# Optimization experiments

Measured on AMD Instinct MI355X. Metric: run time of the kernel, lower is better.

Reference implementation:

```python
import jax, jax.numpy as jnp
import numpy as np

B, L, H = 16, 512, 1024
HEADS, HEAD_SIZE = 12, 64
NEG = 1e12


def sinusoidal_position_embedding(seq_len, output_dim):
    pos = jnp.arange(seq_len, dtype=jnp.float32)[:, None]
    idx = jnp.arange(output_dim // 2, dtype=jnp.float32)
    freqs = pos * jnp.power(10000.0, -2.0 * idx / output_dim)  # [L, D/2]
    emb = jnp.stack([jnp.sin(freqs), jnp.cos(freqs)], axis=-1)  # [L, D/2, 2]
    return emb.reshape(seq_len, output_dim)  # interleaved sin/cos, [L, D]


def setup_inputs() -> dict:
    key = jax.random.key(0)
    k1, k2, k3 = jax.random.split(key, 3)
    inputs = jax.random.normal(k1, (B, L, H), dtype=jnp.float32)
    mask = jnp.ones((B, L), dtype=jnp.int32)
    W = jax.random.normal(k2, (H, HEADS * HEAD_SIZE * 2), dtype=jnp.float32) / np.sqrt(H)
    b = jax.random.normal(k3, (HEADS * HEAD_SIZE * 2,), dtype=jnp.float32) * 0.01
    pos_emb = sinusoidal_position_embedding(L, HEAD_SIZE)  # [L, HEAD_SIZE]
    return {"inputs": inputs, "mask": mask, "W": W, "b": b, "pos_emb": pos_emb}


def rotate_half_interleaved(x):
    # stack([-x[..., 1::2], x[..., ::2]], -1).reshape(x.shape)
    x2 = jnp.stack([-x[..., 1::2], x[..., ::2]], axis=-1)
    return x2.reshape(x.shape)


def reference(inputs, mask, W, b, pos_emb):
    bsz, seq_len, _ = inputs.shape
    d = pos_emb.shape[-1]
    heads = W.shape[1] // (2 * d)
    out = inputs @ W + b                       # [B, L, heads*2d]
    out = out.reshape(bsz, seq_len, heads, 2 * d)
    qw, kw = out[..., :d], out[..., d:]        # [B, L, heads, d]
    cos_pos = jnp.repeat(pos_emb[:, 1::2], 2, axis=-1)[None, :, None, :]  # [1,L,1,d]
    sin_pos = jnp.repeat(pos_emb[:, 0::2], 2, axis=-1)[None, :, None, :]
    qw = qw * cos_pos + rotate_half_interleaved(qw) * sin_pos
    kw = kw * cos_pos + rotate_half_interleaved(kw) * sin_pos
    logits = jnp.einsum('bmhd,bnhd->bhmn', qw, kw)  # [B, heads, L, L]
    pad = mask.astype(logits.dtype)[:, None, None, :] * mask.astype(logits.dtype)[:, None, :, None]
    # torch code: expand of mask[:,None,None,:] -> applies along last axis only;
    # replicate exactly: pad_mask broadcasts mask over the query axis.
    pad_mask = jnp.broadcast_to(mask.astype(logits.dtype)[:, None, None, :], logits.shape)
    logits = logits * pad_mask - (1.0 - pad_mask) * NEG
    tril = jnp.tril(jnp.ones((seq_len, seq_len), dtype=logits.dtype), -1)
    logits = logits - tril[None, None, :, :] * NEG
    return logits / jnp.sqrt(jnp.array(d, dtype=logits.dtype))
```

## Files before the change

kernel.cpp:

```cpp
#include <hip/hip_runtime.h>

#define BB 16
#define LL 512
#define HH 1024
#define HEADS 12
#define DD 64
#define N1 1536
#define M1 8192
#define NEGC 1e12f

typedef short bf16x8 __attribute__((ext_vector_type(8)));
typedef float f32x4 __attribute__((ext_vector_type(4)));

typedef const __attribute__((address_space(1))) unsigned int glob_u32;
typedef __attribute__((address_space(3))) unsigned int lds_u32;

__device__ __forceinline__ void gl_lds16(const unsigned short* g, unsigned short* l) {
    __builtin_amdgcn_global_load_lds((glob_u32*)g, (lds_u32*)l, 16, 0, 0);
}

__device__ __forceinline__ unsigned short f2bf(float f) {
    union { float f; unsigned int u; } v; v.f = f;
    unsigned int u = v.u;
    return (unsigned short)((u + 0x7fffu + ((u >> 16) & 1u)) >> 16);
}

__global__ __launch_bounds__(256) void k_conv_x(const float* __restrict__ X,
                                                unsigned short* __restrict__ Xb,
                                                int n4) {
    int i = blockIdx.x * 256 + threadIdx.x;
    if (i >= n4) return;
    float4 v = ((const float4*)X)[i];
    ushort4 o;
    o.x = f2bf(v.x); o.y = f2bf(v.y); o.z = f2bf(v.z); o.w = f2bf(v.w);
    ((ushort4*)Xb)[i] = o;
}

__global__ __launch_bounds__(256) void k_trans_w(const float* __restrict__ W,
                                                 unsigned short* __restrict__ Wt) {
    __shared__ float tile[32][33];
    int n0 = blockIdx.x * 32;
    int k0 = blockIdx.y * 32;
    int tx = threadIdx.x;
    int ty = threadIdx.y;
#pragma unroll
    for (int i = 0; i < 4; i++) {
        int k = ty + i * 8;
        tile[k][tx] = W[(size_t)(k0 + k) * N1 + n0 + tx];
    }
    __syncthreads();
#pragma unroll
    for (int i = 0; i < 4; i++) {
        int n = ty + i * 8;
        Wt[(size_t)(n0 + n) * HH + k0 + tx] = f2bf(tile[tx][n]);
    }
}

__global__ __launch_bounds__(256) void k_gemm1_rope(
    const unsigned short* __restrict__ Xb,
    const unsigned short* __restrict__ Wt,
    const float* __restrict__ bias,
    const float* __restrict__ pe,
    unsigned short* __restrict__ Qr,
    unsigned short* __restrict__ Kr)
{
    __shared__ __align__(16) unsigned short As[128 * 32];
    __shared__ __align__(16) unsigned short Bs[128 * 32];
    int m0 = blockIdx.y * 128;
    int n0 = blockIdx.x * 128;
    int tid = threadIdx.x;
    int w  = tid >> 6;
    int ln = tid & 63;
    int lq = ln >> 4;
    int lm = ln & 15;
    int wm = (w & 1) * 64;
    int wn = (w >> 1) * 64;

    int lrow = ln >> 2;
    int lcol = (ln & 3) * 8;
    const unsigned short* ga0 = &Xb[(size_t)(m0 + w * 32 + lrow) * HH + lcol];
    const unsigned short* ga1 = ga0 + (size_t)16 * HH;
    const unsigned short* gb0 = &Wt[(size_t)(n0 + w * 32 + lrow) * HH + lcol];
    const unsigned short* gb1 = gb0 + (size_t)16 * HH;
    unsigned short* la0 = &As[(w * 32) * 32];
    unsigned short* la1 = la0 + 16 * 32;
    unsigned short* lb0 = &Bs[(w * 32) * 32];
    unsigned short* lb1 = lb0 + 16 * 32;

    const unsigned short* pa = &As[(wm + lm) * 32];
    const unsigned short* pb = &Bs[(wn + lm) * 32];

    f32x4 acc[4][4] = {};

    for (int kk = 0; kk < HH; kk += 32) {
        gl_lds16(ga0 + kk, la0);
        gl_lds16(ga1 + kk, la1);
        gl_lds16(gb0 + kk, lb0);
        gl_lds16(gb1 + kk, lb1);
        __syncthreads();

        bf16x8 af[4], bf[4];
#pragma unroll
        for (int t = 0; t < 4; t++) {
            af[t] = *(const bf16x8*)&pa[t * 16 * 32 + lq * 8];
            bf[t] = *(const bf16x8*)&pb[t * 16 * 32 + lq * 8];
        }
#pragma unroll
        for (int ti = 0; ti < 4; ti++)
#pragma unroll
            for (int tj = 0; tj < 4; tj++)
                acc[ti][tj] = __builtin_amdgcn_mfma_f32_16x16x32_bf16(af[ti], bf[tj], acc[ti][tj], 0, 0, 0);
        __syncthreads();
    }

#pragma unroll
    for (int tj = 0; tj < 4; tj++) {
        int n = n0 + wn + tj * 16 + lm;
        float bv = bias[n];
        int h = n >> 7;
        int c = n & 127;
        int j = c & 63;
        int ii = j >> 1;
        bool isK = (c >= 64);
        unsigned short* dst = isK ? Kr : Qr;
#pragma unroll
        for (int ti = 0; ti < 4; ti++) {
#pragma unroll
            for (int r = 0; r < 4; r++) {
                int m = m0 + wm + ti * 16 + lq * 4 + r;
                int l = m & (LL - 1);
                int bidx = m >> 9;
                float v = acc[ti][tj][r] + bv;
                float vp = __shfl_xor(v, 1, 64);
                float2 sc = *(const float2*)&pe[l * 64 + 2 * ii];
                float o = (j & 1) ? (v * sc.y + vp * sc.x) : (v * sc.y - vp * sc.x);
                size_t idx = ((size_t)(bidx * HEADS + h) * LL + l) * DD + j;
                dst[idx] = f2bf(o);
            }
        }
    }
}

__global__ __launch_bounds__(256) void k_gemm2(
    const unsigned short* __restrict__ Qr,
    const unsigned short* __restrict__ Kr,
    const int* __restrict__ mask,
    float* __restrict__ out)
{
    __shared__ __align__(16) unsigned short Qs[64 * 72];
    __shared__ __align__(16) unsigned short Ks[64 * 72];
    int bh = blockIdx.z;
    int b  = bh / HEADS;
    int n0 = blockIdx.x * 64;
    int m0 = blockIdx.y * 64;
    int tid = threadIdx.x;
    int w  = tid >> 6;
    int ln = tid & 63;
    int lq = ln >> 4;
    int lm = ln & 15;
    int mw = (w & 1) * 32;
    int nw = (w >> 1) * 32;

    const unsigned short* Qb = Qr + (size_t)bh * LL * DD;
    const unsigned short* Kb = Kr + (size_t)bh * LL * DD;

    int srow = tid >> 3;
    int scol = (tid & 7) * 8;
#pragma unroll
    for (int p = 0; p < 2; p++) {
        int row = srow + p * 32;
        *(uint4*)&Qs[row * 72 + scol] = *(const uint4*)&Qb[(size_t)(m0 + row) * DD + scol];
        *(uint4*)&Ks[row * 72 + scol] = *(const uint4*)&Kb[(size_t)(n0 + row) * DD + scol];
    }
    __syncthreads();

    f32x4 acc[2][2] = {};
#pragma unroll
    for (int kk = 0; kk < 64; kk += 32) {
        bf16x8 q0 = *(const bf16x8*)&Qs[(mw + lm) * 72 + kk + lq * 8];
        bf16x8 q1 = *(const bf16x8*)&Qs[(mw + 16 + lm) * 72 + kk + lq * 8];
        bf16x8 k0 = *(const bf16x8*)&Ks[(nw + lm) * 72 + kk + lq * 8];
        bf16x8 k1 = *(const bf16x8*)&Ks[(nw + 16 + lm) * 72 + kk + lq * 8];
        acc[0][0] = __builtin_amdgcn_mfma_f32_16x16x32_bf16(k0, q0, acc[0][0], 0, 0, 0);
        acc[0][1] = __builtin_amdgcn_mfma_f32_16x16x32_bf16(k1, q0, acc[0][1], 0, 0, 0);
        acc[1][0] = __builtin_amdgcn_mfma_f32_16x16x32_bf16(k0, q1, acc[1][0], 0, 0, 0);
        acc[1][1] = __builtin_amdgcn_mfma_f32_16x16x32_bf16(k1, q1, acc[1][1], 0, 0, 0);
    }

#pragma unroll
    for (int tm = 0; tm < 2; tm++) {
        int m = m0 + mw + tm * 16 + lm;
#pragma unroll
        for (int tn = 0; tn < 2; tn++) {
            int nb = n0 + nw + tn * 16 + lq * 4;
            int4 mv = *(const int4*)&mask[b * LL + nb];
            float4 val;
            {
                float pm = (float)mv.x; int n = nb;
                val.x = (acc[tm][tn][0] * pm - (1.0f - pm) * NEGC - (n < m ? NEGC : 0.0f)) * 0.125f;
            }
            {
                float pm = (float)mv.y; int n = nb + 1;
                val.y = (acc[tm][tn][1] * pm - (1.0f - pm) * NEGC - (n < m ? NEGC : 0.0f)) * 0.125f;
            }
            {
                float pm = (float)mv.z; int n = nb + 2;
                val.z = (acc[tm][tn][2] * pm - (1.0f - pm) * NEGC - (n < m ? NEGC : 0.0f)) * 0.125f;
            }
            {
                float pm = (float)mv.w; int n = nb + 3;
                val.w = (acc[tm][tn][3] * pm - (1.0f - pm) * NEGC - (n < m ? NEGC : 0.0f)) * 0.125f;
            }
            *(float4*)&out[((size_t)bh * LL + m) * LL + nb] = val;
        }
    }
}

extern "C" void kernel_launch(void* const* d_in, const int* in_sizes, int n_in,
                              void* d_out, int out_size, void* d_ws, size_t ws_size,
                              hipStream_t stream) {
    const float* X    = (const float*)d_in[0];
    const int*   mask = (const int*)d_in[1];
    const float* W    = (const float*)d_in[2];
    const float* bias = (const float*)d_in[3];
    const float* pe   = (const float*)d_in[4];
    float* out = (float*)d_out;

    char* ws = (char*)d_ws;
    unsigned short* Xb = (unsigned short*)ws;
    unsigned short* Wt = (unsigned short*)(ws + 16777216);
    unsigned short* Qr = (unsigned short*)(ws + 16777216 + 3145728);
    unsigned short* Kr = Qr + (size_t)BB * HEADS * LL * DD;

    k_conv_x<<<dim3((M1 * HH / 4 + 255) / 256), dim3(256), 0, stream>>>(X, Xb, M1 * HH / 4);
    k_trans_w<<<dim3(N1 / 32, HH / 32), dim3(32, 8), 0, stream>>>(W, Wt);
    k_gemm1_rope<<<dim3(N1 / 128, M1 / 128), dim3(256), 0, stream>>>(Xb, Wt, bias, pe, Qr, Kr);
    k_gemm2<<<dim3(LL / 64, LL / 64, BB * HEADS), dim3(256), 0, stream>>>(Qr, Kr, mask, out);
}
```

Measured before the change: 327.2 us.

## Transpose gemm1 MFMA output for vectorized RoPE stores; enlarge gemm2 tiles to 128x128

In gemm1 the MFMA operands are swapped so each lane holds four consecutive output columns. RoPE pairs can then be rotated within a lane, removing the cross-lane shuffle and the scalar bf16 stores in favour of ushort4 stores with float4 bias and position-embedding loads. In gemm2 the tile grows from 64x64 to 128x128, with each wave computing a 4x4 block of MFMA tiles and the head dimension split into two LDS halves. This cuts the block count and amortizes the mask load over more outputs, at the cost of more registers per thread and fewer blocks in flight.

```diff
diff --git a/kernel.cpp b/kernel.cpp
--- a/kernel.cpp
+++ b/kernel.cpp
@@ -87,8 +87,8 @@
     unsigned short* lb0 = &Bs[(w * 32) * 32];
     unsigned short* lb1 = lb0 + 16 * 32;
 
-    const unsigned short* pa = &As[(wm + lm) * 32];
-    const unsigned short* pb = &Bs[(wn + lm) * 32];
+    const unsigned short* px = &As[(wm + lm) * 32];
+    const unsigned short* pw = &Bs[(wn + lm) * 32];
 
     f32x4 acc[4][4] = {};
 
@@ -99,44 +99,46 @@
         gl_lds16(gb1 + kk, lb1);
         __syncthreads();
 
-        bf16x8 af[4], bf[4];
+        bf16x8 xf[4], wf[4];
 #pragma unroll
         for (int t = 0; t < 4; t++) {
-            af[t] = *(const bf16x8*)&pa[t * 16 * 32 + lq * 8];
-            bf[t] = *(const bf16x8*)&pb[t * 16 * 32 + lq * 8];
+            xf[t] = *(const bf16x8*)&px[t * 16 * 32 + lq * 8];
+            wf[t] = *(const bf16x8*)&pw[t * 16 * 32 + lq * 8];
         }
 #pragma unroll
         for (int ti = 0; ti < 4; ti++)
 #pragma unroll
             for (int tj = 0; tj < 4; tj++)
-                acc[ti][tj] = __builtin_amdgcn_mfma_f32_16x16x32_bf16(af[ti], bf[tj], acc[ti][tj], 0, 0, 0);
+                acc[ti][tj] = __builtin_amdgcn_mfma_f32_16x16x32_bf16(wf[tj], xf[ti], acc[ti][tj], 0, 0, 0);
         __syncthreads();
     }
 
 #pragma unroll
     for (int tj = 0; tj < 4; tj++) {
-        int n = n0 + wn + tj * 16 + lm;
-        float bv = bias[n];
-        int h = n >> 7;
-        int c = n & 127;
-        int j = c & 63;
-        int ii = j >> 1;
+        int nb = n0 + wn + tj * 16 + lq * 4;
+        float4 b4 = *(const float4*)&bias[nb];
+        int h  = nb >> 7;
+        int c  = nb & 127;
+        int jb = c & 63;
         bool isK = (c >= 64);
         unsigned short* dst = isK ? Kr : Qr;
+        size_t hoff = (size_t)h * LL * DD + jb;
 #pragma unroll
         for (int ti = 0; ti < 4; ti++) {
-#pragma unroll
-            for (int r = 0; r < 4; r++) {
-                int m = m0 + wm + ti * 16 + lq * 4 + r;
-                int l = m & (LL - 1);
-                int bidx = m >> 9;
-                float v = acc[ti][tj][r] + bv;
-                float vp = __shfl_xor(v, 1, 64);
-                float2 sc = *(const float2*)&pe[l * 64 + 2 * ii];
-                float o = (j & 1) ? (v * sc.y + vp * sc.x) : (v * sc.y - vp * sc.x);
-                size_t idx = ((size_t)(bidx * HEADS + h) * LL + l) * DD + j;
-                dst[idx] = f2bf(o);
-            }
+            int m = m0 + wm + ti * 16 + lm;
+            int l = m & (LL - 1);
+            int bidx = m >> 9;
+            float4 p4 = *(const float4*)&pe[l * 64 + jb];
+            float v0 = acc[ti][tj][0] + b4.x;
+            float v1 = acc[ti][tj][1] + b4.y;
+            float v2 = acc[ti][tj][2] + b4.z;
+            float v3 = acc[ti][tj][3] + b4.w;
+            ushort4 st;
+            st.x = f2bf(v0 * p4.y - v1 * p4.x);
+            st.y = f2bf(v1 * p4.y + v0 * p4.x);
+            st.z = f2bf(v2 * p4.w - v3 * p4.z);
+            st.w = f2bf(v3 * p4.w + v2 * p4.z);
+            *(ushort4*)&dst[(size_t)bidx * HEADS * LL * DD + hoff + (size_t)l * DD] = st;
         }
     }
 }
@@ -147,70 +149,67 @@
     const int* __restrict__ mask,
     float* __restrict__ out)
 {
-    __shared__ __align__(16) unsigned short Qs[64 * 72];
-    __shared__ __align__(16) unsigned short Ks[64 * 72];
+    __shared__ __align__(16) unsigned short Qs[2][128 * 32];
+    __shared__ __align__(16) unsigned short Ks[2][128 * 32];
     int bh = blockIdx.z;
     int b  = bh / HEADS;
-    int n0 = blockIdx.x * 64;
-    int m0 = blockIdx.y * 64;
+    int n0 = blockIdx.x * 128;
+    int m0 = blockIdx.y * 128;
     int tid = threadIdx.x;
     int w  = tid >> 6;
     int ln = tid & 63;
     int lq = ln >> 4;
     int lm = ln & 15;
-    int mw = (w & 1) * 32;
-    int nw = (w >> 1) * 32;
+    int wm = (w & 1) * 64;
+    int wn = (w >> 1) * 64;
 
     const unsigned short* Qb = Qr + (size_t)bh * LL * DD;
     const unsigned short* Kb = Kr + (size_t)bh * LL * DD;
 
-    int srow = tid >> 3;
-    int scol = (tid & 7) * 8;
+    int row  = tid >> 3;
+    int colq = tid & 7;
+    int pp   = colq >> 2;
+    int cc   = (colq & 3) * 8;
+#pragma unroll
+    for (int rr = 0; rr < 128; rr += 32) {
+        uint4 qv = *(const uint4*)&Qb[(size_t)(m0 + rr + row) * DD + colq * 8];
+        uint4 kv = *(const uint4*)&Kb[(size_t)(n0 + rr + row) * DD + colq * 8];
+        *(uint4*)&Qs[pp][(rr + row) * 32 + cc] = qv;
+        *(uint4*)&Ks[pp][(rr + row) * 32 + cc] = kv;
+    }
+    __syncthreads();
+
+    f32x4 acc[4][4] = {};
 #pragma unroll
     for (int p = 0; p < 2; p++) {
-        int row = srow + p * 32;
-        *(uint4*)&Qs[row * 72 + scol] = *(const uint4*)&Qb[(size_t)(m0 + row) * DD + scol];
-        *(uint4*)&Ks[row * 72 + scol] = *(const uint4*)&Kb[(size_t)(n0 + row) * DD + scol];
-    }
-    __syncthreads();
-
-    f32x4 acc[2][2] = {};
-#pragma unroll
-    for (int kk = 0; kk < 64; kk += 32) {
-        bf16x8 q0 = *(const bf16x8*)&Qs[(mw + lm) * 72 + kk + lq * 8];
-        bf16x8 q1 = *(const bf16x8*)&Qs[(mw + 16 + lm) * 72 + kk + lq * 8];
-        bf16x8 k0 = *(const bf16x8*)&Ks[(nw + lm) * 72 + kk + lq * 8];
-        bf16x8 k1 = *(const bf16x8*)&Ks[(nw + 16 + lm) * 72 + kk + lq * 8];
-        acc[0][0] = __builtin_amdgcn_mfma_f32_16x16x32_bf16(k0, q0, acc[0][0], 0, 0, 0);
-        acc[0][1] = __builtin_amdgcn_mfma_f32_16x16x32_bf16(k1, q0, acc[0][1], 0, 0, 0);
-        acc[1][0] = __builtin_amdgcn_mfma_f32_16x16x32_bf16(k0, q1, acc[1][0], 0, 0, 0);
-        acc[1][1] = __builtin_amdgcn_mfma_f32_16x16x32_bf16(k1, q1, acc[1][1], 0, 0, 0);
-    }
-
-#pragma unroll
-    for (int tm = 0; tm < 2; tm++) {
-        int m = m0 + mw + tm * 16 + lm;
-#pragma unroll
-        for (int tn = 0; tn < 2; tn++) {
-            int nb = n0 + nw + tn * 16 + lq * 4;
-            int4 mv = *(const int4*)&mask[b * LL + nb];
+        bf16x8 kf[4], qf[4];
+#pragma unroll
+        for (int t = 0; t < 4; t++) {
+            kf[t] = *(const bf16x8*)&Ks[p][(wn + t * 16 + lm) * 32 + lq * 8];
+            qf[t] = *(const bf16x8*)&Qs[p][(wm + t * 16 + lm) * 32 + lq * 8];
+        }
+#pragma unroll
+        for (int tm = 0; tm < 4; tm++)
+#pragma unroll
+            for (int tn = 0; tn < 4; tn++)
+                acc[tm][tn] = __builtin_amdgcn_mfma_f32_16x16x32_bf16(kf[tn], qf[tm], acc[tm][tn], 0, 0, 0);
+    }
+
+#pragma unroll
+    for (int tn = 0; tn < 4; tn++) {
+        int nb = n0 + wn + tn * 16 + lq * 4;
+        int4 mv = *(const int4*)&mask[b * LL + nb];
+        float pm0 = (float)mv.x, pm1 = (float)mv.y, pm2 = (float)mv.z, pm3 = (float)mv.w;
+        float ng0 = (1.0f - pm0) * NEGC, ng1 = (1.0f - pm1) * NEGC;
+        float ng2 = (1.0f - pm2) * NEGC, ng3 = (1.0f - pm3) * NEGC;
+#pragma unroll
+        for (int tm = 0; tm < 4; tm++) {
+            int m = m0 + wm + tm * 16 + lm;
             float4 val;
-            {
-                float pm = (float)mv.x; int n = nb;
-                val.x = (acc[tm][tn][0] * pm - (1.0f - pm) * NEGC - (n < m ? NEGC : 0.0f)) * 0.125f;
-            }
-            {
-                float pm = (float)mv.y; int n = nb + 1;
-                val.y = (acc[tm][tn][1] * pm - (1.0f - pm) * NEGC - (n < m ? NEGC : 0.0f)) * 0.125f;
-            }
-            {
-                float pm = (float)mv.z; int n = nb + 2;
-                val.z = (acc[tm][tn][2] * pm - (1.0f - pm) * NEGC - (n < m ? NEGC : 0.0f)) * 0.125f;
-            }
-            {
-                float pm = (float)mv.w; int n = nb + 3;
-                val.w = (acc[tm][tn][3] * pm - (1.0f - pm) * NEGC - (n < m ? NEGC : 0.0f)) * 0.125f;
-            }
+            val.x = (acc[tm][tn][0] * pm0 - ng0 - (nb     < m ? NEGC : 0.0f)) * 0.125f;
+            val.y = (acc[tm][tn][1] * pm1 - ng1 - (nb + 1 < m ? NEGC : 0.0f)) * 0.125f;
+            val.z = (acc[tm][tn][2] * pm2 - ng2 - (nb + 2 < m ? NEGC : 0.0f)) * 0.125f;
+            val.w = (acc[tm][tn][3] * pm3 - ng3 - (nb + 3 < m ? NEGC : 0.0f)) * 0.125f;
             *(float4*)&out[((size_t)bh * LL + m) * LL + nb] = val;
         }
     }
@@ -235,5 +234,5 @@
     k_conv_x<<<dim3((M1 * HH / 4 + 255) / 256), dim3(256), 0, stream>>>(X, Xb, M1 * HH / 4);
     k_trans_w<<<dim3(N1 / 32, HH / 32), dim3(32, 8), 0, stream>>>(W, Wt);
     k_gemm1_rope<<<dim3(N1 / 128, M1 / 128), dim3(256), 0, stream>>>(Xb, Wt, bias, pe, Qr, Kr);
-    k_gemm2<<<dim3(LL / 64, LL / 64, BB * HEADS), dim3(256), 0, stream>>>(Qr, Kr, mask, out);
-}
+    k_gemm2<<<dim3(LL / 128, LL / 128, BB * HEADS), dim3(256), 0, stream>>>(Qr, Kr, mask, out);
+}
```

After: 327.5 us. About the same (+0.1%).
